# Kernel optimization log

Hardware: AMD Instinct MI355X
Metric: run time of the kernel (lower is better)

The kernel has to match this reference:

```python
import jax, jax.numpy as jnp
import numpy as np

B, S, DIM, HEADS = 4, 2048, 1024, 16
SCALE = float((DIM // HEADS) ** 0.5)  # sqrt(d_k) = 8.0
EPS = 1e-5


def _ln(h, g, b):
    m = jnp.mean(h, axis=-1, keepdims=True)
    v = jnp.mean((h - m) ** 2, axis=-1, keepdims=True)
    return (h - m) * jax.lax.rsqrt(v + EPS) * g + b


def setup_inputs() -> dict:
    key = jax.random.key(0)
    ks = jax.random.split(key, 16)
    w = lambda k: jax.random.normal(k, (DIM, DIM), jnp.float32) * 0.02
    vec = lambda k: jax.random.normal(k, (DIM,), jnp.float32) * 0.02
    return {
        "x": jax.random.normal(ks[0], (B, S, DIM), jnp.float32),
        "Wq": w(ks[1]), "bq": vec(ks[2]),
        "Wk": w(ks[3]), "bk": vec(ks[4]),
        "Wv": w(ks[5]), "bv": vec(ks[6]),
        "g_at": 1.0 + vec(ks[7]), "b_at": vec(ks[8]),
        "g_ln": 1.0 + vec(ks[9]), "b_ln": vec(ks[10]),
        "W1": w(ks[11]), "c1": vec(ks[12]),
        "W2": w(ks[13]), "c2": vec(ks[14]),
    }


def reference(x, Wq, bq, Wk, bk, Wv, bv, g_at, b_at, g_ln, b_ln, W1, c1, W2, c2):
    # --- MultiHeadAttention (single-head math: no head reshape in source) ---
    Q = x @ Wq + bq                                   # [B,S,D]
    K = x @ Wk + bk
    V = x @ Wv + bv
    scores = jax.nn.softmax(jnp.einsum('bqd,bkd->bqk', Q, K) / SCALE, axis=-1)
    at = _ln(jnp.einsum('bqk,bkd->bqd', scores, V) + x, g_at, b_at)
    # --- EncoderStack ---
    h = _ln(at + x, g_ln, b_ln)
    res = h
    # note: source's `if i != len(self.ffn)` is always True -> GELU on every layer
    h = jax.nn.gelu(h @ W1 + c1, approximate=False)
    h = jax.nn.gelu(h @ W2 + c2, approximate=False)
    return _ln(h + res, g_ln, b_ln)
```

## Files before the change

kernel.cpp:

```cpp
#include <hip/hip_runtime.h>
#include <cstdint>
#include <cstddef>

#define DIMN 1024
#define SEQ  2048
#define NBAT 4
#define TOKS (NBAT * SEQ)

typedef unsigned short u16;
typedef unsigned int   u32;

typedef __bf16 bf16x8 __attribute__((ext_vector_type(8)));
typedef float  f32x4  __attribute__((ext_vector_type(4)));

#define AS1 __attribute__((address_space(1)))
#define AS3 __attribute__((address_space(3)))


__device__ __forceinline__ u16 f2b(float f) {
  union { float f; u32 u; } v; v.f = f;
  u32 r = v.u + 0x7fffu + ((v.u >> 16) & 1u);
  return (u16)(r >> 16);
}

__device__ __forceinline__ float b2f(u16 b) {
  union { u32 u; float f; } v; v.u = ((u32)b) << 16;
  return v.f;
}

__device__ __forceinline__ float gelu_exact(float v) {
  return 0.5f * v * (1.0f + erff(v * 0.70710678118654752f));
}

__device__ __forceinline__ void blk_sum2(float& a, float& b, float* sm) {
  #pragma unroll
  for (int o = 32; o >= 1; o >>= 1) {
    a += __shfl_xor(a, o, 64);
    b += __shfl_xor(b, o, 64);
  }
  int w = threadIdx.x >> 6;
  if ((threadIdx.x & 63) == 0) { sm[w] = a; sm[4 + w] = b; }
  __syncthreads();
  a = sm[0] + sm[1] + sm[2] + sm[3];
  b = sm[4] + sm[5] + sm[6] + sm[7];
  __syncthreads();
}

__device__ __forceinline__ float blk_max(float a, float* sm) {
  #pragma unroll
  for (int o = 32; o >= 1; o >>= 1) a = fmaxf(a, __shfl_xor(a, o, 64));
  int w = threadIdx.x >> 6;
  if ((threadIdx.x & 63) == 0) sm[w] = a;
  __syncthreads();
  float r = fmaxf(fmaxf(sm[0], sm[1]), fmaxf(sm[2], sm[3]));
  __syncthreads();
  return r;
}

__device__ __forceinline__ float blk_sum1(float a, float* sm) {
  #pragma unroll
  for (int o = 32; o >= 1; o >>= 1) a += __shfl_xor(a, o, 64);
  int w = threadIdx.x >> 6;
  if ((threadIdx.x & 63) == 0) sm[w] = a;
  __syncthreads();
  float r = sm[0] + sm[1] + sm[2] + sm[3];
  __syncthreads();
  return r;
}


__global__ __launch_bounds__(256) void conv_x(const float* __restrict__ x,
                                              u16* __restrict__ xb) {
  size_t i = ((size_t)blockIdx.x * 256 + threadIdx.x) * 4;
  float4 v = *(const float4*)(x + i);
  uint2 o;
  o.x = (u32)f2b(v.x) | ((u32)f2b(v.y) << 16);
  o.y = (u32)f2b(v.z) | ((u32)f2b(v.w) << 16);
  *(uint2*)(xb + i) = o;
}

__global__ __launch_bounds__(256) void transpose_w5(
    const float* __restrict__ Wq, const float* __restrict__ Wk,
    const float* __restrict__ Wv, const float* __restrict__ W1,
    const float* __restrict__ W2,
    u16* __restrict__ Wqkv, u16* __restrict__ W1T, u16* __restrict__ W2T)
{
  const float* W; u16* T;
  switch (blockIdx.z) {
    case 0: W = Wq; T = Wqkv;                      break;
    case 1: W = Wk; T = Wqkv + 1 * DIMN * DIMN;    break;
    case 2: W = Wv; T = Wqkv + 2 * DIMN * DIMN;    break;
    case 3: W = W1; T = W1T;                       break;
    default: W = W2; T = W2T;                      break;
  }
  __shared__ float t[32][33];
  int tx = threadIdx.x, ty = threadIdx.y;
  int k0 = blockIdx.x * 32, n0 = blockIdx.y * 32;
  #pragma unroll
  for (int j = 0; j < 32; j += 8)
    t[ty + j][tx] = W[(size_t)(k0 + ty + j) * DIMN + n0 + tx];
  __syncthreads();
  #pragma unroll
  for (int j = 0; j < 32; j += 8)
    T[(size_t)(n0 + ty + j) * DIMN + k0 + tx] = f2b(t[tx][ty + j]);
}

__global__ __launch_bounds__(256) void transpose_v(const u16* __restrict__ Vb,
                                                   u16* __restrict__ VT) {
  __shared__ u16 t[32][33];
  int tx = threadIdx.x, ty = threadIdx.y;
  int d0 = blockIdx.x * 32, t0 = blockIdx.y * 32;
  const u16* src = Vb + (size_t)blockIdx.z * SEQ * DIMN;
  u16*       dst = VT + (size_t)blockIdx.z * DIMN * SEQ;
  #pragma unroll
  for (int j = 0; j < 32; j += 8)
    t[ty + j][tx] = src[(size_t)(t0 + ty + j) * DIMN + d0 + tx];
  __syncthreads();
  #pragma unroll
  for (int j = 0; j < 32; j += 8)
    dst[(size_t)(d0 + ty + j) * SEQ + t0 + tx] = t[tx][ty + j];
}

template <int EPI, int SWZ>
__global__ __launch_bounds__(256, 2) void gemm128p(
    const u16* __restrict__ A, const u16* __restrict__ Bm,
    u16* __restrict__ Cb, u16* __restrict__ Cb2, u16* __restrict__ Cb3,
    const float* __restrict__ bias, const float* __restrict__ bias2,
    const float* __restrict__ bias3,
    int M, int N, int K, int ldc,
    size_t sA, size_t sB, size_t sC)
{
  __shared__ u16 AB[2][2][2][128 * 32];

  const int tid = threadIdx.x;

  int bm0, bn0;
  if (SWZ == 1) {
    const int id   = blockIdx.y * gridDim.x + blockIdx.x;
    const int xcd  = id & 7;
    const int idx  = id >> 3;
    const int band = gridDim.x >> 3;
    const int bm_l = idx % band;
    const int bn   = idx / band;
    bm0 = (xcd * band + bm_l) * 128;
    bn0 = bn * 128;
  } else {
    bm0 = blockIdx.x * 128;
    bn0 = blockIdx.y * 128;
  }

  A  += (size_t)blockIdx.z * sA;
  Bm += (size_t)blockIdx.z * sB;

  const int wave = tid >> 6, lane = tid & 63;
  const int wm   = (wave >> 1) * 64, wn = (wave & 1) * 64;
  const int l16  = lane & 15, quad = lane >> 4;
  const int rs8  = (quad ^ ((l16 >> 1) & 3)) << 3;
  const int cg8  = ((lane & 3) ^ ((lane >> 3) & 3)) << 3;
  const int srow = wave * 32 + (lane >> 2);

  f32x4 acc[4][4] = {};
  bf16x8 af[4], bf[4];

  const int nk = K >> 6;

#define VM4() asm volatile("s_waitcnt vmcnt(4)" ::: "memory")
#define VM0() asm volatile("s_waitcnt vmcnt(0)" ::: "memory")
#define SBAR() __builtin_amdgcn_s_barrier()

#define STG(BUF, KH, KT) do {                                                  \
    const int _kc = (KT) * 64 + (KH) * 32;                                     \
    _Pragma("unroll")                                                          \
    for (int _j = 0; _j < 2; ++_j) {                                           \
      const u16* _gA = A  + (size_t)(bm0 + srow + _j * 16) * K + _kc + cg8;    \
      const u16* _gB = Bm + (size_t)(bn0 + srow + _j * 16) * K + _kc + cg8;    \
      u16* _lA = &AB[BUF][0][KH][(wave * 128 + _j * 64) * 8];                  \
      u16* _lB = &AB[BUF][1][KH][(wave * 128 + _j * 64) * 8];                  \
      __builtin_amdgcn_global_load_lds((const AS1 void*)_gA, (AS3 void*)_lA,   \
                                       16, 0, 0);                              \
      __builtin_amdgcn_global_load_lds((const AS1 void*)_gB, (AS3 void*)_lB,   \
                                       16, 0, 0);                              \
    }                                                                          \
  } while (0)

#define LDA(BUF, KH) do {                                                      \
    const u16* _u = &AB[BUF][0][KH][0];                                        \
    _Pragma("unroll")                                                          \
    for (int _i = 0; _i < 4; ++_i)                                             \
      af[_i] = *(const bf16x8*)(_u + (wm + _i * 16 + l16) * 32 + rs8);         \
  } while (0)

#define LDB(BUF, KH) do {                                                      \
    const u16* _u = &AB[BUF][1][KH][0];                                        \
    _Pragma("unroll")                                                          \
    for (int _i = 0; _i < 4; ++_i)                                             \
      bf[_i] = *(const bf16x8*)(_u + (wn + _i * 16 + l16) * 32 + rs8);         \
  } while (0)

#define MMCL() do {                                                            \
    __builtin_amdgcn_s_setprio(1);                                             \
    _Pragma("unroll")                                                          \
    for (int _mt = 0; _mt < 4; ++_mt) {                                        \
      _Pragma("unroll")                                                        \
      for (int _nt = 0; _nt < 4; ++_nt)                                        \
        acc[_mt][_nt] = __builtin_amdgcn_mfma_f32_16x16x32_bf16(               \
            af[_mt], bf[_nt], acc[_mt][_nt], 0, 0, 0);                         \
    }                                                                          \
    __builtin_amdgcn_s_setprio(0);                                             \
  } while (0)

  STG(0, 0, 0);
  STG(0, 1, 0);
  VM4(); SBAR();

  for (int t = 0; t < nk; ++t) {
    const int buf = t & 1, nb = buf ^ 1;
    const bool last = (t == nk - 1);

    LDA(buf, 0); LDB(buf, 0);
    if (!last) STG(nb, 0, t + 1);
    MMCL();
    if (last) VM0(); else VM4();
    SBAR();

    LDA(buf, 1); LDB(buf, 1);
    if (!last) STG(nb, 1, t + 1);
    MMCL();
    if (!last) { VM4(); }
    SBAR();
  }

#undef VM4
#undef VM0
#undef SBAR
#undef STG
#undef LDA
#undef LDB
#undef MMCL

  u16* Cbz = Cb + (size_t)blockIdx.z * sC;

  #pragma unroll
  for (int mt = 0; mt < 4; ++mt) {
    int grow0 = bm0 + wm + mt * 16 + quad * 4;
    #pragma unroll
    for (int nt = 0; nt < 4; ++nt) {
      int gcol = bn0 + wn + nt * 16 + l16;
      if (EPI == 3) {
        const int seg = gcol >> 10;
        const int col = gcol & 1023;
        const float* bp = (seg == 0) ? bias : (seg == 1) ? bias2 : bias3;
        u16*         cp = (seg == 0) ? Cb   : (seg == 1) ? Cb2   : Cb3;
        float bv = bp[col];
        #pragma unroll
        for (int r = 0; r < 4; ++r)
          cp[(size_t)(grow0 + r) * ldc + col] = f2b(acc[mt][nt][r] + bv);
      } else if (EPI == 4) {
        float bv = bias[gcol];
        #pragma unroll
        for (int r = 0; r < 4; ++r)
          Cbz[(size_t)(grow0 + r) * ldc + gcol] =
              f2b(gelu_exact(acc[mt][nt][r] + bv));
      } else {
        #pragma unroll
        for (int r = 0; r < 4; ++r)
          Cbz[(size_t)(grow0 + r) * ldc + gcol] = f2b(acc[mt][nt][r]);
      }
    }
  }
}

template <int EPI, int SWZ>
__global__ __launch_bounds__(512, 2) void gemm256(
    const u16* __restrict__ A, const u16* __restrict__ Bm,
    u16* __restrict__ Cb, u16* __restrict__ Cb2, u16* __restrict__ Cb3,
    const float* __restrict__ bias, const float* __restrict__ bias2,
    const float* __restrict__ bias3,
    int M, int N, int K, int ldc,
    size_t sA, size_t sB, size_t sC)
{
  __shared__ u16 AB[2][2][2][256 * 32];

  const int tid = threadIdx.x;

  int bm0, bn0;
  if (SWZ == 1) {
    const int id   = blockIdx.y * gridDim.x + blockIdx.x;
    const int xcd  = id & 7;
    const int idx  = id >> 3;
    const int band = gridDim.x >> 3;
    const int bm_l = idx % band;
    const int bn   = idx / band;
    bm0 = (xcd * band + bm_l) * 256;
    bn0 = bn * 256;
  } else {
    bm0 = blockIdx.x * 256;
    bn0 = blockIdx.y * 256;
  }

  A  += (size_t)blockIdx.z * sA;
  Bm += (size_t)blockIdx.z * sB;

  const int wave = tid >> 6, lane = tid & 63;
  const int wm   = (wave >> 2) * 128, wn = (wave & 3) * 64;
  const int l16  = lane & 15, quad = lane >> 4;
  const int rs8  = (quad ^ ((l16 >> 1) & 3)) << 3;
  const int cg8  = ((lane & 3) ^ ((lane >> 3) & 3)) << 3;
  const int srow = wave * 32 + (lane >> 2);

  f32x4 acc[8][4] = {};
  bf16x8 af[4], bf[4];

  const int nk  = K >> 6;
  const int nit = nk >> 1;

#define VM8() asm volatile("s_waitcnt vmcnt(8)" ::: "memory")
#define VM4() asm volatile("s_waitcnt vmcnt(4)" ::: "memory")
#define VM0() asm volatile("s_waitcnt vmcnt(0)" ::: "memory")
#define SBAR() __builtin_amdgcn_s_barrier()

#define STG(BUF, ABI, KH, KT) do {                                             \
    const u16* _P   = (ABI) ? Bm : A;                                          \
    const int _b0   = (ABI) ? bn0 : bm0;                                       \
    const int _kc   = (KT) * 64 + (KH) * 32;                                   \
    _Pragma("unroll")                                                          \
    for (int _j = 0; _j < 2; ++_j) {                                           \
      const u16* _g = _P + (size_t)(_b0 + srow + _j * 16) * K + _kc + cg8;     \
      u16* _l = &AB[BUF][ABI][KH][(wave * 128 + _j * 64) * 8];                 \
      __builtin_amdgcn_global_load_lds((const AS1 void*)_g, (AS3 void*)_l,     \
                                       16, 0, 0);                              \
    }                                                                          \
  } while (0)

#define LDA(BUF, KH, MH) do {                                                  \
    const u16* _u = &AB[BUF][0][KH][0];                                        \
    _Pragma("unroll")                                                          \
    for (int _i = 0; _i < 4; ++_i)                                             \
      af[_i] = *(const bf16x8*)(_u + (wm + (MH) * 64 + _i * 16 + l16) * 32     \
                                  + rs8);                                      \
  } while (0)

#define LDB(BUF, KH) do {                                                      \
    const u16* _u = &AB[BUF][1][KH][0];                                        \
    _Pragma("unroll")                                                          \
    for (int _i = 0; _i < 4; ++_i)                                             \
      bf[_i] = *(const bf16x8*)(_u + (wn + _i * 16 + l16) * 32 + rs8);         \
  } while (0)

#define MMCL(MH) do {                                                          \
    __builtin_amdgcn_s_setprio(1);                                             \
    _Pragma("unroll")                                                          \
    for (int _mt = 0; _mt < 4; ++_mt) {                                        \
      _Pragma("unroll")                                                        \
      for (int _nt = 0; _nt < 4; ++_nt)                                        \
        acc[(MH) * 4 + _mt][_nt] = __builtin_amdgcn_mfma_f32_16x16x32_bf16(    \
            af[_mt], bf[_nt], acc[(MH) * 4 + _mt][_nt], 0, 0, 0);              \
    }                                                                          \
    __builtin_amdgcn_s_setprio(0);                                             \
  } while (0)

  STG(0, 0, 0, 0); STG(0, 1, 0, 0);
  STG(0, 0, 1, 0); STG(0, 1, 1, 0);
  STG(1, 0, 0, 1); STG(1, 1, 0, 1);
  VM8(); SBAR();

  for (int i = 0; i < nit; ++i) {
    const int t1 = 2 * i + 1;
    const bool last = (i == nit - 1);

    LDA(0, 0, 0); LDB(0, 0);
    STG(1, 0, 1, t1);
    SBAR();
    MMCL(0);
    SBAR();

    LDA(0, 0, 1);
    STG(1, 1, 1, t1);
    SBAR();
    MMCL(1);
    VM8(); SBAR();

    LDA(0, 1, 0); LDB(0, 1);
    if (!last) STG(0, 0, 0, t1 + 1);
    SBAR();
    MMCL(0);
    SBAR();

    LDA(0, 1, 1);
    if (!last) STG(0, 1, 0, t1 + 1);
    SBAR();
    MMCL(1);
    if (last) VM4(); else VM8();
    SBAR();

    LDA(1, 0, 0); LDB(1, 0);
    if (!last) STG(0, 0, 1, t1 + 1);
    SBAR();
    MMCL(0);
    SBAR();

    LDA(1, 0, 1);
    if (!last) STG(0, 1, 1, t1 + 1);
    SBAR();
    MMCL(1);
    if (last) VM0(); else VM8();
    SBAR();

    LDA(1, 1, 0); LDB(1, 1);
    if (!last) STG(1, 0, 0, t1 + 2);
    SBAR();
    MMCL(0);
    SBAR();

    LDA(1, 1, 1);
    if (!last) STG(1, 1, 0, t1 + 2);
    SBAR();
    MMCL(1);
    if (!last) { VM8(); }
    SBAR();
  }

#undef VM8
#undef VM4
#undef VM0
#undef SBAR
#undef STG
#undef LDA
#undef LDB
#undef MMCL

  u16* Cbz = Cb + (size_t)blockIdx.z * sC;

  #pragma unroll
  for (int mt = 0; mt < 8; ++mt) {
    int grow0 = bm0 + wm + mt * 16 + quad * 4;
    #pragma unroll
    for (int nt = 0; nt < 4; ++nt) {
      int gcol = bn0 + wn + nt * 16 + l16;
      if (EPI == 3) {
        const int seg = gcol >> 10;
        const int col = gcol & 1023;
        const float* bp = (seg == 0) ? bias : (seg == 1) ? bias2 : bias3;
        u16*         cp = (seg == 0) ? Cb   : (seg == 1) ? Cb2   : Cb3;
        float bv = bp[col];
        #pragma unroll
        for (int r = 0; r < 4; ++r)
          cp[(size_t)(grow0 + r) * ldc + col] = f2b(acc[mt][nt][r] + bv);
      } else if (EPI == 4) {
        float bv = bias[gcol];
        #pragma unroll
        for (int r = 0; r < 4; ++r)
          Cbz[(size_t)(grow0 + r) * ldc + gcol] =
              f2b(gelu_exact(acc[mt][nt][r] + bv));
      } else {
        #pragma unroll
        for (int r = 0; r < 4; ++r)
          Cbz[(size_t)(grow0 + r) * ldc + gcol] = f2b(acc[mt][nt][r]);
      }
    }
  }
}

__global__ __launch_bounds__(256) void softmax_rows(const u16* __restrict__ Sc,
                                                    u16* __restrict__ P) {
  __shared__ float sm[8];
  int row = blockIdx.x, t = threadIdx.x;
  const u16* s = Sc + (size_t)row * SEQ;
  uint4 raw = *(const uint4*)(s + t * 8);
  float v[8];
  #pragma unroll
  for (int m = 0; m < 4; ++m) {
    u32 w = ((const u32*)&raw)[m];
    v[2 * m]     = b2f((u16)(w & 0xffff)) * 0.125f;
    v[2 * m + 1] = b2f((u16)(w >> 16)) * 0.125f;
  }
  float mx = -1e30f;
  #pragma unroll
  for (int i = 0; i < 8; ++i) mx = fmaxf(mx, v[i]);
  mx = blk_max(mx, sm);
  float sum = 0.0f;
  #pragma unroll
  for (int i = 0; i < 8; ++i) { v[i] = __expf(v[i] - mx); sum += v[i]; }
  sum = blk_sum1(sum, sm);
  float inv = 1.0f / sum;
  uint4 o;
  #pragma unroll
  for (int m = 0; m < 4; ++m)
    ((u32*)&o)[m] = (u32)f2b(v[2 * m] * inv) | ((u32)f2b(v[2 * m + 1] * inv) << 16);
  *(uint4*)(P + (size_t)row * SEQ + t * 8) = o;
}

__global__ __launch_bounds__(256) void ln1_fused(
    const u16* __restrict__ attn, const u16* __restrict__ xb,
    const float* __restrict__ g_at, const float* __restrict__ b_at,
    const float* __restrict__ g_ln, const float* __restrict__ b_ln,
    u16* __restrict__ hres)
{
  __shared__ float sm[8];
  int row = blockIdx.x, t = threadIdx.x;
  size_t base = (size_t)row * DIMN;
  uint2 ar = *(const uint2*)(attn + base + t * 4);
  uint2 xr4 = *(const uint2*)(xb + base + t * 4);
  float y[4], xr[4];
  float s = 0.0f, s2 = 0.0f;
  #pragma unroll
  for (int i = 0; i < 4; ++i) {
    u32 aw = ((const u32*)&ar)[i >> 1];
    u32 xw = ((const u32*)&xr4)[i >> 1];
    float av = b2f((u16)((i & 1) ? (aw >> 16) : (aw & 0xffff)));
    xr[i]    = b2f((u16)((i & 1) ? (xw >> 16) : (xw & 0xffff)));
    y[i] = av + xr[i];
    s += y[i]; s2 += y[i] * y[i];
  }
  blk_sum2(s, s2, sm);
  float m  = s * (1.0f / DIMN);
  float rs = rsqrtf(s2 * (1.0f / DIMN) - m * m + 1e-5f);
  float z[4];
  s = 0.0f; s2 = 0.0f;
  #pragma unroll
  for (int i = 0; i < 4; ++i) {
    int c = t * 4 + i;
    float at = (y[i] - m) * rs * g_at[c] + b_at[c];
    z[i] = at + xr[i];
    s += z[i]; s2 += z[i] * z[i];
  }
  blk_sum2(s, s2, sm);
  float m2  = s * (1.0f / DIMN);
  float rs2 = rsqrtf(s2 * (1.0f / DIMN) - m2 * m2 + 1e-5f);
  uint2 o;
  #pragma unroll
  for (int i = 0; i < 2; ++i) {
    int c = t * 4 + 2 * i;
    float h0 = (z[2 * i]     - m2) * rs2 * g_ln[c]     + b_ln[c];
    float h1 = (z[2 * i + 1] - m2) * rs2 * g_ln[c + 1] + b_ln[c + 1];
    ((u32*)&o)[i] = (u32)f2b(h0) | ((u32)f2b(h1) << 16);
  }
  *(uint2*)(hres + base + t * 4) = o;
}

__global__ __launch_bounds__(256) void ln2_final(
    const u16* __restrict__ u, const u16* __restrict__ hres,
    const float* __restrict__ g, const float* __restrict__ bb,
    float* __restrict__ out)
{
  __shared__ float sm[8];
  int row = blockIdx.x, t = threadIdx.x;
  size_t base = (size_t)row * DIMN;
  uint2 ur = *(const uint2*)(u + base + t * 4);
  uint2 hr = *(const uint2*)(hres + base + t * 4);
  float y[4];
  float s = 0.0f, s2 = 0.0f;
  #pragma unroll
  for (int i = 0; i < 4; ++i) {
    u32 uw = ((const u32*)&ur)[i >> 1];
    u32 hw = ((const u32*)&hr)[i >> 1];
    float uv = b2f((u16)((i & 1) ? (uw >> 16) : (uw & 0xffff)));
    float hv = b2f((u16)((i & 1) ? (hw >> 16) : (hw & 0xffff)));
    y[i] = uv + hv;
    s += y[i]; s2 += y[i] * y[i];
  }
  blk_sum2(s, s2, sm);
  float m  = s * (1.0f / DIMN);
  float rs = rsqrtf(s2 * (1.0f / DIMN) - m * m + 1e-5f);
  float4 o;
  o.x = (y[0] - m) * rs * g[t * 4 + 0] + bb[t * 4 + 0];
  o.y = (y[1] - m) * rs * g[t * 4 + 1] + bb[t * 4 + 1];
  o.z = (y[2] - m) * rs * g[t * 4 + 2] + bb[t * 4 + 2];
  o.w = (y[3] - m) * rs * g[t * 4 + 3] + bb[t * 4 + 3];
  *(float4*)(out + base + t * 4) = o;
}


extern "C" void kernel_launch(void* const* d_in, const int* in_sizes, int n_in,
                              void* d_out, int out_size, void* d_ws, size_t ws_size,
                              hipStream_t stream)
{
  const float* x    = (const float*)d_in[0];
  const float* Wq   = (const float*)d_in[1];
  const float* bq   = (const float*)d_in[2];
  const float* Wk   = (const float*)d_in[3];
  const float* bk   = (const float*)d_in[4];
  const float* Wv   = (const float*)d_in[5];
  const float* bv   = (const float*)d_in[6];
  const float* g_at = (const float*)d_in[7];
  const float* b_at = (const float*)d_in[8];
  const float* g_ln = (const float*)d_in[9];
  const float* b_ln = (const float*)d_in[10];
  const float* W1   = (const float*)d_in[11];
  const float* c1   = (const float*)d_in[12];
  const float* W2   = (const float*)d_in[13];
  const float* c2   = (const float*)d_in[14];
  float* out = (float*)d_out;

  char* ws = (char*)d_ws;
  const size_t MB = 1u << 20;
  u16* xb    = (u16*)(ws + 0 * MB);
  u16* W1T   = (u16*)(ws + 16 * MB);
  u16* W2T   = (u16*)(ws + 18 * MB);
  u16* WqkvT = (u16*)(ws + 20 * MB);
  u16* Qb    = (u16*)(ws + 26 * MB);
  u16* Kb    = (u16*)(ws + 42 * MB);
  u16* Vb    = (u16*)(ws + 58 * MB);
  u16* VT    = (u16*)(ws + 74 * MB);
  u16* Sc    = (u16*)(ws + 90 * MB);
  u16* attn  = (u16*)(ws + 90 * MB);
  u16* hres  = (u16*)(ws + 106 * MB);
  u16* Pb    = (u16*)(ws + 122 * MB);
  u16* tb    = Kb;
  u16* ub    = Vb;

  conv_x<<<(TOKS * DIMN) / 1024, 256, 0, stream>>>(x, xb);
  transpose_w5<<<dim3(32, 32, 5), dim3(32, 8), 0, stream>>>(
      Wq, Wk, Wv, W1, W2, WqkvT, W1T, W2T);

  gemm256<3, 1><<<dim3(32, 12), 512, 0, stream>>>(
      xb, WqkvT, Qb, Kb, Vb, bq, bk, bv,
      TOKS, 3 * DIMN, DIMN, DIMN, 0, 0, 0);

  transpose_v<<<dim3(32, 64, NBAT), dim3(32, 8), 0, stream>>>(Vb, VT);

  gemm256<6, 0><<<dim3(8, 8, NBAT), 512, 0, stream>>>(
      Qb, Kb, Sc, nullptr, nullptr, nullptr, nullptr, nullptr,
      SEQ, SEQ, DIMN, SEQ,
      (size_t)SEQ * DIMN, (size_t)SEQ * DIMN, (size_t)SEQ * SEQ);
  softmax_rows<<<TOKS, 256, 0, stream>>>(Sc, Pb);

  gemm128p<6, 0><<<dim3(16, 8, NBAT), 256, 0, stream>>>(
      Pb, VT, attn, nullptr, nullptr, nullptr, nullptr, nullptr,
      SEQ, DIMN, SEQ, DIMN,
      (size_t)SEQ * SEQ, (size_t)DIMN * SEQ, (size_t)SEQ * DIMN);

  ln1_fused<<<TOKS, 256, 0, stream>>>(attn, xb, g_at, b_at, g_ln, b_ln, hres);

  gemm128p<4, 1><<<dim3(64, 8), 256, 0, stream>>>(
      hres, W1T, tb, nullptr, nullptr, c1, nullptr, nullptr,
      TOKS, DIMN, DIMN, DIMN, 0, 0, 0);
  gemm128p<4, 1><<<dim3(64, 8), 256, 0, stream>>>(
      tb, W2T, ub, nullptr, nullptr, c2, nullptr, nullptr,
      TOKS, DIMN, DIMN, DIMN, 0, 0, 0);

  ln2_final<<<TOKS, 256, 0, stream>>>(ub, hres, g_ln, b_ln, out);
}
```

Measured before the change: 362.6 us.

## Double-buffer LDS fragment registers to overlap ds_reads with MFMA in both GEMMs

Both GEMM kernels now hold two sets of A/B register fragments. The next K-half's LDS reads are issued before the current MFMA cluster, and the prefetch distance of global-to-LDS staging is extended, so LDS latency hides behind matrix math. The 256-tile kernel also drops roughly half of its barriers and retunes its vmcnt waits. In exchange it uses more VGPRs, which may lower occupancy, and the reworked barrier and wait placement carries a risk of LDS read/write races.

```diff
diff --git a/kernel.cpp b/kernel.cpp
--- a/kernel.cpp
+++ b/kernel.cpp
@@ -160,7 +160,7 @@
   const int srow = wave * 32 + (lane >> 2);
 
   f32x4 acc[4][4] = {};
-  bf16x8 af[4], bf[4];
+  bf16x8 af0[4], bf0[4], af1[4], bf1[4];
 
   const int nk = K >> 6;
 
@@ -183,50 +183,49 @@
     }                                                                          \
   } while (0)
 
-#define LDA(BUF, KH) do {                                                      \
-    const u16* _u = &AB[BUF][0][KH][0];                                        \
+#define LDR(AF, BF, BUF, KH) do {                                              \
+    const u16* _ua = &AB[BUF][0][KH][0];                                       \
+    const u16* _ub = &AB[BUF][1][KH][0];                                       \
     _Pragma("unroll")                                                          \
     for (int _i = 0; _i < 4; ++_i)                                             \
-      af[_i] = *(const bf16x8*)(_u + (wm + _i * 16 + l16) * 32 + rs8);         \
+      AF[_i] = *(const bf16x8*)(_ua + (wm + _i * 16 + l16) * 32 + rs8);        \
+    _Pragma("unroll")                                                          \
+    for (int _i = 0; _i < 4; ++_i)                                             \
+      BF[_i] = *(const bf16x8*)(_ub + (wn + _i * 16 + l16) * 32 + rs8);        \
   } while (0)
 
-#define LDB(BUF, KH) do {                                                      \
-    const u16* _u = &AB[BUF][1][KH][0];                                        \
-    _Pragma("unroll")                                                          \
-    for (int _i = 0; _i < 4; ++_i)                                             \
-      bf[_i] = *(const bf16x8*)(_u + (wn + _i * 16 + l16) * 32 + rs8);         \
-  } while (0)
-
-#define MMCL() do {                                                            \
+#define MMCL(AF, BF) do {                                                      \
     __builtin_amdgcn_s_setprio(1);                                             \
     _Pragma("unroll")                                                          \
     for (int _mt = 0; _mt < 4; ++_mt) {                                        \
       _Pragma("unroll")                                                        \
       for (int _nt = 0; _nt < 4; ++_nt)                                        \
         acc[_mt][_nt] = __builtin_amdgcn_mfma_f32_16x16x32_bf16(               \
-            af[_mt], bf[_nt], acc[_mt][_nt], 0, 0, 0);                         \
+            AF[_mt], BF[_nt], acc[_mt][_nt], 0, 0, 0);                         \
     }                                                                          \
     __builtin_amdgcn_s_setprio(0);                                             \
   } while (0)
 
   STG(0, 0, 0);
   STG(0, 1, 0);
+  STG(1, 0, 1);
   VM4(); SBAR();
+  LDR(af0, bf0, 0, 0);
 
   for (int t = 0; t < nk; ++t) {
     const int buf = t & 1, nb = buf ^ 1;
-    const bool last = (t == nk - 1);
-
-    LDA(buf, 0); LDB(buf, 0);
-    if (!last) STG(nb, 0, t + 1);
-    MMCL();
-    if (last) VM0(); else VM4();
-    SBAR();
-
-    LDA(buf, 1); LDB(buf, 1);
-    if (!last) STG(nb, 1, t + 1);
-    MMCL();
-    if (!last) { VM4(); }
+
+    if (t + 1 < nk) STG(nb, 1, t + 1);
+    LDR(af1, bf1, buf, 1);
+    MMCL(af0, bf0);
+    if (t + 1 < nk) VM4();
+    SBAR();
+
+    if (t + 2 < nk) STG(buf, 0, t + 2);
+    if (t + 1 < nk) LDR(af0, bf0, nb, 0);
+    MMCL(af1, bf1);
+    if (t + 2 < nk) { VM4(); }
+    else if (t + 1 < nk) { VM0(); }
     SBAR();
   }
 
@@ -234,8 +233,7 @@
 #undef VM0
 #undef SBAR
 #undef STG
-#undef LDA
-#undef LDB
+#undef LDR
 #undef MMCL
 
   u16* Cbz = Cb + (size_t)blockIdx.z * sC;
@@ -309,12 +307,13 @@
   const int srow = wave * 32 + (lane >> 2);
 
   f32x4 acc[8][4] = {};
-  bf16x8 af[4], bf[4];
+  bf16x8 af0[4], af1[4], bf0[4], bf1[4];
 
   const int nk  = K >> 6;
   const int nit = nk >> 1;
 
 #define VM8() asm volatile("s_waitcnt vmcnt(8)" ::: "memory")
+#define VM6() asm volatile("s_waitcnt vmcnt(6)" ::: "memory")
 #define VM4() asm volatile("s_waitcnt vmcnt(4)" ::: "memory")
 #define VM0() asm volatile("s_waitcnt vmcnt(0)" ::: "memory")
 #define SBAR() __builtin_amdgcn_s_barrier()
@@ -332,29 +331,29 @@
     }                                                                          \
   } while (0)
 
-#define LDA(BUF, KH, MH) do {                                                  \
+#define LDA_TO(DST, BUF, KH, MH) do {                                          \
     const u16* _u = &AB[BUF][0][KH][0];                                        \
     _Pragma("unroll")                                                          \
     for (int _i = 0; _i < 4; ++_i)                                             \
-      af[_i] = *(const bf16x8*)(_u + (wm + (MH) * 64 + _i * 16 + l16) * 32     \
-                                  + rs8);                                      \
+      DST[_i] = *(const bf16x8*)(_u + (wm + (MH) * 64 + _i * 16 + l16) * 32    \
+                                   + rs8);                                     \
   } while (0)
 
-#define LDB(BUF, KH) do {                                                      \
+#define LDB_TO(DST, BUF, KH) do {                                              \
     const u16* _u = &AB[BUF][1][KH][0];                                        \
     _Pragma("unroll")                                                          \
     for (int _i = 0; _i < 4; ++_i)                                             \
-      bf[_i] = *(const bf16x8*)(_u + (wn + _i * 16 + l16) * 32 + rs8);         \
+      DST[_i] = *(const bf16x8*)(_u + (wn + _i * 16 + l16) * 32 + rs8);        \
   } while (0)
 
-#define MMCL(MH) do {                                                          \
+#define MMCL(AF, BF, MH) do {                                                  \
     __builtin_amdgcn_s_setprio(1);                                             \
     _Pragma("unroll")                                                          \
     for (int _mt = 0; _mt < 4; ++_mt) {                                        \
       _Pragma("unroll")                                                        \
       for (int _nt = 0; _nt < 4; ++_nt)                                        \
         acc[(MH) * 4 + _mt][_nt] = __builtin_amdgcn_mfma_f32_16x16x32_bf16(    \
-            af[_mt], bf[_nt], acc[(MH) * 4 + _mt][_nt], 0, 0, 0);              \
+            AF[_mt], BF[_nt], acc[(MH) * 4 + _mt][_nt], 0, 0, 0);              \
     }                                                                          \
     __builtin_amdgcn_s_setprio(0);                                             \
   } while (0)
@@ -363,70 +362,67 @@
   STG(0, 0, 1, 0); STG(0, 1, 1, 0);
   STG(1, 0, 0, 1); STG(1, 1, 0, 1);
   VM8(); SBAR();
+  LDA_TO(af0, 0, 0, 0); LDB_TO(bf0, 0, 0);
 
   for (int i = 0; i < nit; ++i) {
     const int t1 = 2 * i + 1;
     const bool last = (i == nit - 1);
 
-    LDA(0, 0, 0); LDB(0, 0);
     STG(1, 0, 1, t1);
-    SBAR();
-    MMCL(0);
-    SBAR();
-
-    LDA(0, 0, 1);
+    LDA_TO(af1, 0, 0, 1);
+    MMCL(af0, bf0, 0);
+    VM6();
+    SBAR();
+
     STG(1, 1, 1, t1);
-    SBAR();
-    MMCL(1);
-    VM8(); SBAR();
-
-    LDA(0, 1, 0); LDB(0, 1);
+    LDA_TO(af0, 0, 1, 0); LDB_TO(bf1, 0, 1);
+    MMCL(af1, bf0, 1);
+    SBAR();
+
     if (!last) STG(0, 0, 0, t1 + 1);
-    SBAR();
-    MMCL(0);
-    SBAR();
-
-    LDA(0, 1, 1);
+    LDA_TO(af1, 0, 1, 1);
+    MMCL(af0, bf1, 0);
+    if (last) VM4(); else VM6();
+    SBAR();
+
     if (!last) STG(0, 1, 0, t1 + 1);
-    SBAR();
-    MMCL(1);
-    if (last) VM4(); else VM8();
-    SBAR();
-
-    LDA(1, 0, 0); LDB(1, 0);
+    LDA_TO(af0, 1, 0, 0); LDB_TO(bf0, 1, 0);
+    MMCL(af1, bf1, 1);
+    SBAR();
+
     if (!last) STG(0, 0, 1, t1 + 1);
-    SBAR();
-    MMCL(0);
-    SBAR();
-
-    LDA(1, 0, 1);
+    LDA_TO(af1, 1, 0, 1);
+    MMCL(af0, bf0, 0);
+    if (last) VM0(); else VM6();
+    SBAR();
+
     if (!last) STG(0, 1, 1, t1 + 1);
-    SBAR();
-    MMCL(1);
-    if (last) VM0(); else VM8();
-    SBAR();
-
-    LDA(1, 1, 0); LDB(1, 1);
+    LDA_TO(af0, 1, 1, 0); LDB_TO(bf1, 1, 1);
+    MMCL(af1, bf0, 1);
+    SBAR();
+
     if (!last) STG(1, 0, 0, t1 + 2);
-    SBAR();
-    MMCL(0);
-    SBAR();
-
-    LDA(1, 1, 1);
-    if (!last) STG(1, 1, 0, t1 + 2);
-    SBAR();
-    MMCL(1);
-    if (!last) { VM8(); }
+    LDA_TO(af1, 1, 1, 1);
+    MMCL(af0, bf1, 0);
+    if (!last) VM6();
+    SBAR();
+
+    if (!last) {
+      STG(1, 1, 0, t1 + 2);
+      LDA_TO(af0, 0, 0, 0); LDB_TO(bf0, 0, 0);
+    }
+    MMCL(af1, bf1, 1);
     SBAR();
   }
 
 #undef VM8
+#undef VM6
 #undef VM4
 #undef VM0
 #undef SBAR
 #undef STG
-#undef LDA
-#undef LDB
+#undef LDA_TO
+#undef LDB_TO
 #undef MMCL
 
   u16* Cbz = Cb + (size_t)blockIdx.z * sC;
```

Result: no change. 368.7 us (+1.7%).

## Switch 128-tile GEMM to 32x32x16 MFMA and use it for QKV projection

Applied to the files above, without the earlier changes.

The 128x128 GEMM kernel now has each wave compute its 64x64 sub-tile with 2x2 32x32x16 bf16 MFMAs instead of 4x4 16x16x32 ones. That changes the LDS fragment loads and swizzle offsets, and the epilogue row mapping for the 16-element accumulators. The larger MFMA shape cuts LDS fragment reads per FLOP and the instruction count. The fused QKV projection also moves from the 256-tile kernel to this 128-tile kernel with a larger grid, which risks lower data reuse per block but gives more blocks to spread across CUs.

```diff
diff --git a/kernel.cpp b/kernel.cpp
--- a/kernel.cpp
+++ b/kernel.cpp
@@ -12,6 +12,7 @@
 
 typedef __bf16 bf16x8 __attribute__((ext_vector_type(8)));
 typedef float  f32x4  __attribute__((ext_vector_type(4)));
+typedef float  f32x16 __attribute__((ext_vector_type(16)));
 
 #define AS1 __attribute__((address_space(1)))
 #define AS3 __attribute__((address_space(3)))
@@ -122,7 +123,7 @@
 }
 
 template <int EPI, int SWZ>
-__global__ __launch_bounds__(256, 2) void gemm128p(
+__global__ __launch_bounds__(256, 2) void gemm128w(
     const u16* __restrict__ A, const u16* __restrict__ Bm,
     u16* __restrict__ Cb, u16* __restrict__ Cb2, u16* __restrict__ Cb3,
     const float* __restrict__ bias, const float* __restrict__ bias2,
@@ -154,13 +155,15 @@
 
   const int wave = tid >> 6, lane = tid & 63;
   const int wm   = (wave >> 1) * 64, wn = (wave & 1) * 64;
-  const int l16  = lane & 15, quad = lane >> 4;
-  const int rs8  = (quad ^ ((l16 >> 1) & 3)) << 3;
+  const int l31  = lane & 31, kg = lane >> 5;
+  const int sw32 = (l31 >> 1) & 3;
+  const int rof0 = ((0 + kg) ^ sw32) << 3;
+  const int rof1 = ((2 + kg) ^ sw32) << 3;
   const int cg8  = ((lane & 3) ^ ((lane >> 3) & 3)) << 3;
   const int srow = wave * 32 + (lane >> 2);
 
-  f32x4 acc[4][4] = {};
-  bf16x8 af[4], bf[4];
+  f32x16 acc[2][2] = {};
+  bf16x8 afr[2][2], bfr[2][2];
 
   const int nk = K >> 6;
 
@@ -183,28 +186,32 @@
     }                                                                          \
   } while (0)
 
-#define LDA(BUF, KH) do {                                                      \
-    const u16* _u = &AB[BUF][0][KH][0];                                        \
-    _Pragma("unroll")                                                          \
-    for (int _i = 0; _i < 4; ++_i)                                             \
-      af[_i] = *(const bf16x8*)(_u + (wm + _i * 16 + l16) * 32 + rs8);         \
+#define LDR32(BUF, KH) do {                                                    \
+    const u16* _ua = &AB[BUF][0][KH][0];                                       \
+    const u16* _ub = &AB[BUF][1][KH][0];                                       \
+    _Pragma("unroll")                                                          \
+    for (int _mt = 0; _mt < 2; ++_mt) {                                        \
+      afr[_mt][0] = *(const bf16x8*)(_ua + (wm + _mt * 32 + l31) * 32 + rof0); \
+      afr[_mt][1] = *(const bf16x8*)(_ua + (wm + _mt * 32 + l31) * 32 + rof1); \
+    }                                                                          \
+    _Pragma("unroll")                                                          \
+    for (int _nt = 0; _nt < 2; ++_nt) {                                        \
+      bfr[_nt][0] = *(const bf16x8*)(_ub + (wn + _nt * 32 + l31) * 32 + rof0); \
+      bfr[_nt][1] = *(const bf16x8*)(_ub + (wn + _nt * 32 + l31) * 32 + rof1); \
+    }                                                                          \
   } while (0)
 
-#define LDB(BUF, KH) do {                                                      \
-    const u16* _u = &AB[BUF][1][KH][0];                                        \
-    _Pragma("unroll")                                                          \
-    for (int _i = 0; _i < 4; ++_i)                                             \
-      bf[_i] = *(const bf16x8*)(_u + (wn + _i * 16 + l16) * 32 + rs8);         \
-  } while (0)
-
-#define MMCL() do {                                                            \
+#define MMCL32() do {                                                          \
     __builtin_amdgcn_s_setprio(1);                                             \
     _Pragma("unroll")                                                          \
-    for (int _mt = 0; _mt < 4; ++_mt) {                                        \
+    for (int _f = 0; _f < 2; ++_f) {                                           \
       _Pragma("unroll")                                                        \
-      for (int _nt = 0; _nt < 4; ++_nt)                                        \
-        acc[_mt][_nt] = __builtin_amdgcn_mfma_f32_16x16x32_bf16(               \
-            af[_mt], bf[_nt], acc[_mt][_nt], 0, 0, 0);                         \
+      for (int _mt = 0; _mt < 2; ++_mt) {                                      \
+        _Pragma("unroll")                                                      \
+        for (int _nt = 0; _nt < 2; ++_nt)                                      \
+          acc[_mt][_nt] = __builtin_amdgcn_mfma_f32_32x32x16_bf16(             \
+              afr[_mt][_f], bfr[_nt][_f], acc[_mt][_nt], 0, 0, 0);             \
+      }                                                                        \
     }                                                                          \
     __builtin_amdgcn_s_setprio(0);                                             \
   } while (0)
@@ -217,15 +224,15 @@
     const int buf = t & 1, nb = buf ^ 1;
     const bool last = (t == nk - 1);
 
-    LDA(buf, 0); LDB(buf, 0);
+    LDR32(buf, 0);
     if (!last) STG(nb, 0, t + 1);
-    MMCL();
+    MMCL32();
     if (last) VM0(); else VM4();
     SBAR();
 
-    LDA(buf, 1); LDB(buf, 1);
+    LDR32(buf, 1);
     if (!last) STG(nb, 1, t + 1);
-    MMCL();
+    MMCL32();
     if (!last) { VM4(); }
     SBAR();
   }
@@ -234,18 +241,17 @@
 #undef VM0
 #undef SBAR
 #undef STG
-#undef LDA
-#undef LDB
-#undef MMCL
+#undef LDR32
+#undef MMCL32
 
   u16* Cbz = Cb + (size_t)blockIdx.z * sC;
 
   #pragma unroll
-  for (int mt = 0; mt < 4; ++mt) {
-    int grow0 = bm0 + wm + mt * 16 + quad * 4;
+  for (int mt = 0; mt < 2; ++mt) {
+    int grow_b = bm0 + wm + mt * 32;
     #pragma unroll
-    for (int nt = 0; nt < 4; ++nt) {
-      int gcol = bn0 + wn + nt * 16 + l16;
+    for (int nt = 0; nt < 2; ++nt) {
+      int gcol = bn0 + wn + nt * 32 + l31;
       if (EPI == 3) {
         const int seg = gcol >> 10;
         const int col = gcol & 1023;
@@ -253,18 +259,23 @@
         u16*         cp = (seg == 0) ? Cb   : (seg == 1) ? Cb2   : Cb3;
         float bv = bp[col];
         #pragma unroll
-        for (int r = 0; r < 4; ++r)
-          cp[(size_t)(grow0 + r) * ldc + col] = f2b(acc[mt][nt][r] + bv);
+        for (int r = 0; r < 16; ++r) {
+          int grow = grow_b + (r & 3) + 8 * (r >> 2) + 4 * kg;
+          cp[(size_t)grow * ldc + col] = f2b(acc[mt][nt][r] + bv);
+        }
       } else if (EPI == 4) {
         float bv = bias[gcol];
         #pragma unroll
-        for (int r = 0; r < 4; ++r)
-          Cbz[(size_t)(grow0 + r) * ldc + gcol] =
-              f2b(gelu_exact(acc[mt][nt][r] + bv));
+        for (int r = 0; r < 16; ++r) {
+          int grow = grow_b + (r & 3) + 8 * (r >> 2) + 4 * kg;
+          Cbz[(size_t)grow * ldc + gcol] = f2b(gelu_exact(acc[mt][nt][r] + bv));
+        }
       } else {
         #pragma unroll
-        for (int r = 0; r < 4; ++r)
-          Cbz[(size_t)(grow0 + r) * ldc + gcol] = f2b(acc[mt][nt][r]);
+        for (int r = 0; r < 16; ++r) {
+          int grow = grow_b + (r & 3) + 8 * (r >> 2) + 4 * kg;
+          Cbz[(size_t)grow * ldc + gcol] = f2b(acc[mt][nt][r]);
+        }
       }
     }
   }
@@ -613,7 +624,7 @@
   transpose_w5<<<dim3(32, 32, 5), dim3(32, 8), 0, stream>>>(
       Wq, Wk, Wv, W1, W2, WqkvT, W1T, W2T);
 
-  gemm256<3, 1><<<dim3(32, 12), 512, 0, stream>>>(
+  gemm128w<3, 1><<<dim3(64, 24), 256, 0, stream>>>(
       xb, WqkvT, Qb, Kb, Vb, bq, bk, bv,
       TOKS, 3 * DIMN, DIMN, DIMN, 0, 0, 0);
 
@@ -625,17 +636,17 @@
       (size_t)SEQ * DIMN, (size_t)SEQ * DIMN, (size_t)SEQ * SEQ);
   softmax_rows<<<TOKS, 256, 0, stream>>>(Sc, Pb);
 
-  gemm128p<6, 0><<<dim3(16, 8, NBAT), 256, 0, stream>>>(
+  gemm128w<6, 0><<<dim3(16, 8, NBAT), 256, 0, stream>>>(
       Pb, VT, attn, nullptr, nullptr, nullptr, nullptr, nullptr,
       SEQ, DIMN, SEQ, DIMN,
       (size_t)SEQ * SEQ, (size_t)DIMN * SEQ, (size_t)SEQ * DIMN);
 
   ln1_fused<<<TOKS, 256, 0, stream>>>(attn, xb, g_at, b_at, g_ln, b_ln, hres);
 
-  gemm128p<4, 1><<<dim3(64, 8), 256, 0, stream>>>(
+  gemm128w<4, 1><<<dim3(64, 8), 256, 0, stream>>>(
       hres, W1T, tb, nullptr, nullptr, c1, nullptr, nullptr,
       TOKS, DIMN, DIMN, DIMN, 0, 0, 0);
-  gemm128p<4, 1><<<dim3(64, 8), 256, 0, stream>>>(
+  gemm128w<4, 1><<<dim3(64, 8), 256, 0, stream>>>(
       tb, W2T, ub, nullptr, nullptr, c2, nullptr, nullptr,
       TOKS, DIMN, DIMN, DIMN, 0, 0, 0);
 
```

New measurement: 374.3 us. +3.2%, slower.

## Restructure 128-tile GEMM into triple-buffered K=32 pipeline and use it for QKV

Applied to the files above, without the earlier changes.

The 128x128 GEMM drops its double-buffered 64-wide K stages for a three-slot ring of 32-wide K tiles. Loads run two tiles ahead with one barrier per step, shared memory shrinks from 64KB to 48KB, and launch bounds rise to 3 blocks per CU. The fused QKV projection also moves from the 256-tile kernel to this one with a 64x24 grid, trading per-block reuse for more occupancy and latency hiding. Barriers per unit of K stay the same, but each MFMA cluster between barriers is now smaller.

```diff
diff --git a/kernel.cpp b/kernel.cpp
--- a/kernel.cpp
+++ b/kernel.cpp
@@ -122,7 +122,7 @@
 }
 
 template <int EPI, int SWZ>
-__global__ __launch_bounds__(256, 2) void gemm128p(
+__global__ __launch_bounds__(256, 3) void gemm128q(
     const u16* __restrict__ A, const u16* __restrict__ Bm,
     u16* __restrict__ Cb, u16* __restrict__ Cb2, u16* __restrict__ Cb3,
     const float* __restrict__ bias, const float* __restrict__ bias2,
@@ -130,7 +130,7 @@
     int M, int N, int K, int ldc,
     size_t sA, size_t sB, size_t sC)
 {
-  __shared__ u16 AB[2][2][2][128 * 32];
+  __shared__ u16 AB[3][2][128 * 32];
 
   const int tid = threadIdx.x;
 
@@ -162,20 +162,20 @@
   f32x4 acc[4][4] = {};
   bf16x8 af[4], bf[4];
 
-  const int nk = K >> 6;
+  const int nk = K >> 5;
 
 #define VM4() asm volatile("s_waitcnt vmcnt(4)" ::: "memory")
 #define VM0() asm volatile("s_waitcnt vmcnt(0)" ::: "memory")
 #define SBAR() __builtin_amdgcn_s_barrier()
 
-#define STG(BUF, KH, KT) do {                                                  \
-    const int _kc = (KT) * 64 + (KH) * 32;                                     \
+#define STG(BUF, KT) do {                                                      \
+    const int _kc = (KT) * 32;                                                 \
     _Pragma("unroll")                                                          \
     for (int _j = 0; _j < 2; ++_j) {                                           \
       const u16* _gA = A  + (size_t)(bm0 + srow + _j * 16) * K + _kc + cg8;    \
       const u16* _gB = Bm + (size_t)(bn0 + srow + _j * 16) * K + _kc + cg8;    \
-      u16* _lA = &AB[BUF][0][KH][(wave * 128 + _j * 64) * 8];                  \
-      u16* _lB = &AB[BUF][1][KH][(wave * 128 + _j * 64) * 8];                  \
+      u16* _lA = &AB[BUF][0][(wave * 128 + _j * 64) * 8];                      \
+      u16* _lB = &AB[BUF][1][(wave * 128 + _j * 64) * 8];                      \
       __builtin_amdgcn_global_load_lds((const AS1 void*)_gA, (AS3 void*)_lA,   \
                                        16, 0, 0);                              \
       __builtin_amdgcn_global_load_lds((const AS1 void*)_gB, (AS3 void*)_lB,   \
@@ -183,18 +183,15 @@
     }                                                                          \
   } while (0)
 
-#define LDA(BUF, KH) do {                                                      \
-    const u16* _u = &AB[BUF][0][KH][0];                                        \
+#define LDR(BUF) do {                                                          \
+    const u16* _ua = &AB[BUF][0][0];                                           \
+    const u16* _ub = &AB[BUF][1][0];                                           \
     _Pragma("unroll")                                                          \
     for (int _i = 0; _i < 4; ++_i)                                             \
-      af[_i] = *(const bf16x8*)(_u + (wm + _i * 16 + l16) * 32 + rs8);         \
-  } while (0)
-
-#define LDB(BUF, KH) do {                                                      \
-    const u16* _u = &AB[BUF][1][KH][0];                                        \
+      af[_i] = *(const bf16x8*)(_ua + (wm + _i * 16 + l16) * 32 + rs8);        \
     _Pragma("unroll")                                                          \
     for (int _i = 0; _i < 4; ++_i)                                             \
-      bf[_i] = *(const bf16x8*)(_u + (wn + _i * 16 + l16) * 32 + rs8);         \
+      bf[_i] = *(const bf16x8*)(_ub + (wn + _i * 16 + l16) * 32 + rs8);        \
   } while (0)
 
 #define MMCL() do {                                                            \
@@ -209,24 +206,18 @@
     __builtin_amdgcn_s_setprio(0);                                             \
   } while (0)
 
-  STG(0, 0, 0);
-  STG(0, 1, 0);
+  STG(0, 0);
+  STG(1, 1);
   VM4(); SBAR();
 
   for (int t = 0; t < nk; ++t) {
-    const int buf = t & 1, nb = buf ^ 1;
-    const bool last = (t == nk - 1);
-
-    LDA(buf, 0); LDB(buf, 0);
-    if (!last) STG(nb, 0, t + 1);
+    const int b = t % 3;
+
+    LDR(b);
+    if (t + 2 < nk) STG((t + 2) % 3, t + 2);
     MMCL();
-    if (last) VM0(); else VM4();
-    SBAR();
-
-    LDA(buf, 1); LDB(buf, 1);
-    if (!last) STG(nb, 1, t + 1);
-    MMCL();
-    if (!last) { VM4(); }
+    if (t + 2 < nk) { VM4(); }
+    else if (t + 1 < nk) { VM0(); }
     SBAR();
   }
 
@@ -234,8 +225,7 @@
 #undef VM0
 #undef SBAR
 #undef STG
-#undef LDA
-#undef LDB
+#undef LDR
 #undef MMCL
 
   u16* Cbz = Cb + (size_t)blockIdx.z * sC;
@@ -613,7 +603,7 @@
   transpose_w5<<<dim3(32, 32, 5), dim3(32, 8), 0, stream>>>(
       Wq, Wk, Wv, W1, W2, WqkvT, W1T, W2T);
 
-  gemm256<3, 1><<<dim3(32, 12), 512, 0, stream>>>(
+  gemm128q<3, 1><<<dim3(64, 24), 256, 0, stream>>>(
       xb, WqkvT, Qb, Kb, Vb, bq, bk, bv,
       TOKS, 3 * DIMN, DIMN, DIMN, 0, 0, 0);
 
@@ -625,17 +615,17 @@
       (size_t)SEQ * DIMN, (size_t)SEQ * DIMN, (size_t)SEQ * SEQ);
   softmax_rows<<<TOKS, 256, 0, stream>>>(Sc, Pb);
 
-  gemm128p<6, 0><<<dim3(16, 8, NBAT), 256, 0, stream>>>(
+  gemm128q<6, 0><<<dim3(16, 8, NBAT), 256, 0, stream>>>(
       Pb, VT, attn, nullptr, nullptr, nullptr, nullptr, nullptr,
       SEQ, DIMN, SEQ, DIMN,
       (size_t)SEQ * SEQ, (size_t)DIMN * SEQ, (size_t)SEQ * DIMN);
 
   ln1_fused<<<TOKS, 256, 0, stream>>>(attn, xb, g_at, b_at, g_ln, b_ln, hres);
 
-  gemm128p<4, 1><<<dim3(64, 8), 256, 0, stream>>>(
+  gemm128q<4, 1><<<dim3(64, 8), 256, 0, stream>>>(
       hres, W1T, tb, nullptr, nullptr, c1, nullptr, nullptr,
       TOKS, DIMN, DIMN, DIMN, 0, 0, 0);
-  gemm128p<4, 1><<<dim3(64, 8), 256, 0, stream>>>(
+  gemm128q<4, 1><<<dim3(64, 8), 256, 0, stream>>>(
       tb, W2T, ub, nullptr, nullptr, c2, nullptr, nullptr,
       TOKS, DIMN, DIMN, DIMN, 0, 0, 0);
 
```

Measured after the change: 372.6 us. 2.7% more time.
